# Optimization experiments

Hardware: AMD Instinct MI355X
Metric: run time of the kernel (lower is better)

## Reference

```python
import jax, jax.numpy as jnp
import numpy as np
import math

# dims
BSZ, L, D = 2, 4096, 1024
EXPAND, DS, NH, NG, DC, CS = 2, 128, 32, 1, 4, 64
DI = EXPAND * D            # 2048
HP = DI // NH              # 64 headdim
D_IN_PROJ = 2 * DI + 2 * NG * DS + NH  # 4384
CONV_DIM = DI + 2 * NG * DS            # 2304
EPS = 1e-5


def setup_inputs() -> dict:
    key = jax.random.key(0)
    ks = jax.random.split(key, 10)
    u = jax.random.normal(ks[0], (BSZ, L, D), dtype=jnp.float32)
    W_in = jax.random.normal(ks[1], (D, D_IN_PROJ), dtype=jnp.float32) / math.sqrt(D)
    conv_w = jax.random.normal(ks[2], (CONV_DIM, DC), dtype=jnp.float32) / math.sqrt(DC)
    conv_b = jnp.zeros((CONV_DIM,), dtype=jnp.float32)
    # dt init as in module: dt ~ logspace(1e-3, 0.1), dt_bias = inv softplus
    dt = jnp.exp(jax.random.uniform(ks[3], (NH,)) * (math.log(0.1) - math.log(0.001)) + math.log(0.001))
    dt = jnp.clip(dt, 1e-4, None)
    dt_bias = dt + jnp.log(-jnp.expm1(-dt))
    A_log = jnp.log(jax.random.uniform(ks[4], (NH,), minval=1.0, maxval=16.0))
    norm_w = jnp.ones((DI,), dtype=jnp.float32)
    norm_b = jnp.zeros((DI,), dtype=jnp.float32)
    W_out = jax.random.normal(ks[5], (DI, D), dtype=jnp.float32) / math.sqrt(DI)
    return {"u": u, "W_in": W_in, "conv_w": conv_w, "conv_b": conv_b,
            "dt_bias": dt_bias, "A_log": A_log, "norm_w": norm_w,
            "norm_b": norm_b, "W_out": W_out}


def _segsum(x):
    # x: (..., l) -> (..., l, l), out[i,j] = sum_{j<t<=i} x[t], -inf above diag
    cs = jnp.cumsum(x, axis=-1)
    d = cs[..., :, None] - cs[..., None, :]
    n = x.shape[-1]
    mask = jnp.tril(jnp.ones((n, n), dtype=bool))
    return jnp.where(mask, d, -jnp.inf)


def _ssd(x, A, Bm, Cm):
    # x: (b,l,h,p) already scaled by dt; A: (b,l,h) = a*dt; Bm,Cm: (b,l,h,n)
    b, l, h, p = x.shape
    nc = l // CS
    x = x.reshape(b, nc, CS, h, p)
    A = A.reshape(b, nc, CS, h).transpose(0, 3, 1, 2)          # (b,h,c,s)
    Bm = Bm.reshape(b, nc, CS, h, -1)
    Cm = Cm.reshape(b, nc, CS, h, -1)
    A_cum = jnp.cumsum(A, axis=-1)                              # (b,h,c,s)
    Lmat = jnp.exp(_segsum(A))                                  # (b,h,c,s,s)
    # intra-chunk (diagonal block) output
    Yd = jnp.einsum('bclhn,bcshn,bhcls,bcshp->bclhp', Cm, Bm, Lmat, x)
    # per-chunk final states
    decay_states = jnp.exp(A_cum[..., -1:] - A_cum)             # (b,h,c,s)
    states = jnp.einsum('bcshn,bhcs,bcshp->bchpn', Bm, decay_states, x)
    # inter-chunk recurrence (parallel via segsum over chunk decays)
    A_chunk = jnp.pad(A_cum[..., -1], ((0, 0), (0, 0), (1, 0)))  # (b,h,c+1)
    decay_chunk = jnp.exp(_segsum(A_chunk))                      # (b,h,c+1,c+1)
    states0 = jnp.concatenate([jnp.zeros_like(states[:, :1]), states], axis=1)
    new_states = jnp.einsum('bhzc,bchpn->bzhpn', decay_chunk, states0)
    states_in = new_states[:, :-1]                               # (b,c,h,p,n)
    state_decay = jnp.exp(A_cum)                                 # (b,h,c,s)
    Yoff = jnp.einsum('bcshn,bchpn,bhcs->bcshp', Cm, states_in, state_decay)
    return (Yd + Yoff).reshape(b, l, h, p)


def _causal_dwconv(x, w, b):
    # x: (B,L,C), depthwise causal conv, kernel w: (C,K), bias b: (C,)
    k = w.shape[1]
    xp = jnp.pad(x, ((0, 0), (k - 1, 0), (0, 0)))
    seqlen = x.shape[1]
    out = b
    for i in range(k):  # small fixed kernel loop (K=4)
        out = out + xp[:, i:i + seqlen, :] * w[:, i]
    return out


def reference(u, W_in, conv_w, conv_b, dt_bias, A_log, norm_w, norm_b, W_out):
    b, l, _ = u.shape
    zxbcdt = u @ W_in                                  # (b,l,2*DI+2*NG*DS+NH)
    z = zxbcdt[..., :DI]
    xBC = zxbcdt[..., DI:DI + CONV_DIM]
    dt = jax.nn.softplus(zxbcdt[..., -NH:] + dt_bias)  # (b,l,h)
    A = -jnp.exp(A_log)                                # (h,)
    xBC = jax.nn.silu(_causal_dwconv(xBC, conv_w, conv_b))
    x = xBC[..., :DI].reshape(b, l, NH, HP)
    Bv = xBC[..., DI:DI + NG * DS].reshape(b, l, NG, DS)
    Cv = xBC[..., DI + NG * DS:].reshape(b, l, NG, DS)
    # broadcast groups to heads
    rep = NH // NG
    Bh = jnp.repeat(Bv, rep, axis=2)                   # (b,l,h,n)
    Ch = jnp.repeat(Cv, rep, axis=2)
    y = _ssd(x * dt[..., None], A * dt, Bh, Ch)        # (b,l,h,p)
    y = y.reshape(b, l, DI)
    y = y * jax.nn.silu(z)                             # gated
    mu = jnp.mean(y, axis=-1, keepdims=True)
    var = jnp.mean(jnp.square(y - mu), axis=-1, keepdims=True)
    y = (y - mu) * jax.lax.rsqrt(var + EPS) * norm_w + norm_b
    return y @ W_out
```

## Files before the change

### kernel.cpp

```cpp
#include <hip/hip_runtime.h>
#include <hip/hip_bf16.h>
#include <math.h>


namespace {

constexpr int kB   = 2;
constexpr int kL   = 4096;
constexpr int kDI  = 2048;
constexpr int kDS  = 128;
constexpr int kNH  = 32;
constexpr int kHP  = 64;
constexpr int kDC  = 4;
constexpr int kCS  = 64;
constexpr int kNC  = kL / kCS;
constexpr int kDProj   = 2 * kDI + 2 * kDS + kNH;
constexpr int kDProjP  = 4480;
constexpr int kConvDim = kDI + 2 * kDS;
constexpr int kRows = kB * kL;
constexpr float kEps = 1e-5f;
constexpr int kTS = 130;
constexpr int kWS = 68;

typedef __bf16 bf16x8 __attribute__((ext_vector_type(8)));
typedef float f32x4 __attribute__((ext_vector_type(4)));
typedef unsigned short ushort8 __attribute__((ext_vector_type(8)));

__device__ inline float bu2f(unsigned short u) {
  union { unsigned int i; float f; } x; x.i = ((unsigned int)u) << 16; return x.f;
}
__device__ inline unsigned short f2bu(float f) {
  __hip_bfloat16 h = __float2bfloat16(f);
  return *reinterpret_cast<unsigned short*>(&h);
}

__device__ inline void gld_lds16(const unsigned short* g, unsigned short* l) {
  __builtin_amdgcn_global_load_lds(
      (const __attribute__((address_space(1))) unsigned int*)g,
      (__attribute__((address_space(3))) unsigned int*)l, 16, 0, 0);
}

__global__ void prep_kernel(const float4* __restrict__ u4, ushort4* __restrict__ A1,
                            const float* __restrict__ W_in, unsigned short* __restrict__ Bt1,
                            const float* __restrict__ W_out, unsigned short* __restrict__ Bt2,
                            const float* __restrict__ norm_w, const float* __restrict__ norm_b,
                            float* __restrict__ t1, float* __restrict__ t2) {
  constexpr int kCastBlocks = kRows * 1024 / 4 / 256;
  constexpr int kT1X = kDProjP / 32;
  constexpr int kT1Blocks = kT1X * (1024 / 32);
  constexpr int kT2X = 1024 / 32;
  constexpr int kT2Blocks = kT2X * (2048 / 32);
  __shared__ float t[32][33];
  __shared__ float p1[4][64], p2[4][64];
  int bid = (int)blockIdx.x;
  const int tid = threadIdx.x;
  if (bid < kCastBlocks) {
    int i = bid * 256 + tid;
    float4 v = u4[i];
    ushort4 o;
    o.x = f2bu(v.x); o.y = f2bu(v.y); o.z = f2bu(v.z); o.w = f2bu(v.w);
    A1[i] = o;
    return;
  }
  bid -= kCastBlocks;
  if (bid < kT1Blocks + kT2Blocks) {
    const float* in;
    unsigned short* out;
    int R, C, bx, by;
    const float* scale;
    if (bid < kT1Blocks) {
      in = W_in; out = Bt1; R = 1024; C = kDProj; scale = nullptr;
      bx = bid % kT1X; by = bid / kT1X;
    } else {
      int r = bid - kT1Blocks;
      in = W_out; out = Bt2; R = 2048; C = 1024; scale = norm_w;
      bx = r % kT2X; by = r / kT2X;
    }
    const int c0 = bx * 32, r0 = by * 32;
    const int tx = tid & 31, ty = tid >> 5;
    for (int rr = ty; rr < 32; rr += 8) {
      int c = c0 + tx;
      float v = (c < C) ? in[(size_t)(r0 + rr) * C + c] : 0.f;
      if (scale) v *= scale[r0 + rr];
      t[rr][tx] = v;
    }
    __syncthreads();
    for (int cc = ty; cc < 32; cc += 8) {
      int orow = c0 + cc;
      out[(size_t)orow * R + r0 + tx] = f2bu(t[tx][cc]);
    }
    return;
  }
  bid -= kT1Blocks + kT2Blocks;
  {
    const int nl = tid & 63;
    const int ks = tid >> 6;
    const int n = bid * 64 + nl;
    float s1 = 0.f, s2 = 0.f;
    for (int k = ks * 512; k < ks * 512 + 512; k++) {
      float v = W_out[(size_t)k * 1024 + n];
      s1 += norm_w[k] * v;
      s2 += norm_b[k] * v;
    }
    p1[ks][nl] = s1; p2[ks][nl] = s2;
    __syncthreads();
    if (tid < 64) {
      t1[bid * 64 + tid] = p1[0][tid] + p1[1][tid] + p1[2][tid] + p1[3][tid];
      t2[bid * 64 + tid] = p2[0][tid] + p2[1][tid] + p2[2][tid] + p2[3][tid];
    }
  }
}

__global__ __launch_bounds__(256, 4) void gemm_in(const unsigned short* __restrict__ A,
                                                  const unsigned short* __restrict__ Bt,
                                                  unsigned short* __restrict__ C,
                                                  int M, int N, int K) {
  __shared__ __align__(16) unsigned short As[128 * 64];
  __shared__ __align__(16) unsigned short Bs[128 * 64];
  const int tid = threadIdx.x;
  const int wave = tid >> 6, lane = tid & 63;
  const int nwg = (int)(gridDim.x * gridDim.y);
  const int orig = (int)(blockIdx.y * gridDim.x + blockIdx.x);
  const int swz = (orig & 7) * (nwg >> 3) + (orig >> 3);
  const int bx = swz % (int)gridDim.x, by = swz / (int)gridDim.x;
  const int m0 = by * 128, n0 = bx * 128;
  const int wr = (wave >> 1) * 64, wc = (wave & 1) * 64;
  const int l8 = lane >> 3, s8 = lane & 7;
  const unsigned short* pA[4];
  const unsigned short* pB[4];
  unsigned short* lA[4];
  unsigned short* lB[4];
#pragma unroll
  for (int r = 0; r < 4; r++) {
    int q = wave * 4 + r;
    pA[r] = A + (size_t)(m0 + q * 8 + l8) * K + (s8 ^ l8) * 8;
    pB[r] = Bt + (size_t)(n0 + q * 8 + l8) * K + (s8 ^ l8) * 8;
    lA[r] = &As[q * 512];
    lB[r] = &Bs[q * 512];
  }
  const int fr = lane & 15;
  const int c4 = lane >> 4;
  const int sk0 = (c4 ^ (fr & 7)) * 8;
  const int sk1 = ((4 | c4) ^ (fr & 7)) * 8;
  f32x4 acc[4][4] = {};
  for (int k0 = 0; k0 < K; k0 += 64) {
#pragma unroll
    for (int r = 0; r < 4; r++) {
      gld_lds16(pA[r] + k0, lA[r]);
      gld_lds16(pB[r] + k0, lB[r]);
    }
    asm volatile("s_waitcnt vmcnt(0)" ::: "memory");
    __syncthreads();
    {
      bf16x8 af0[4], bf0[4];
#pragma unroll
      for (int i = 0; i < 4; i++) {
        af0[i] = *(const bf16x8*)&As[(wr + i * 16 + fr) * 64 + sk0];
        bf0[i] = *(const bf16x8*)&Bs[(wc + i * 16 + fr) * 64 + sk0];
      }
#pragma unroll
      for (int i = 0; i < 4; i++)
#pragma unroll
        for (int j = 0; j < 4; j++)
          acc[i][j] = __builtin_amdgcn_mfma_f32_16x16x32_bf16(af0[i], bf0[j], acc[i][j], 0, 0, 0);
    }
    {
      bf16x8 af1[4], bf1[4];
#pragma unroll
      for (int i = 0; i < 4; i++) {
        af1[i] = *(const bf16x8*)&As[(wr + i * 16 + fr) * 64 + sk1];
        bf1[i] = *(const bf16x8*)&Bs[(wc + i * 16 + fr) * 64 + sk1];
      }
#pragma unroll
      for (int i = 0; i < 4; i++)
#pragma unroll
        for (int j = 0; j < 4; j++)
          acc[i][j] = __builtin_amdgcn_mfma_f32_16x16x32_bf16(af1[i], bf1[j], acc[i][j], 0, 0, 0);
    }
    __syncthreads();
  }
  const int crow = (lane >> 4) * 4;
  const int ccol = lane & 15;
#pragma unroll
  for (int i = 0; i < 4; i++) {
#pragma unroll
    for (int j = 0; j < 4; j++) {
      int n = n0 + wc + j * 16 + ccol;
      if (n < N) {
#pragma unroll
        for (int r = 0; r < 4; r++) {
          int m = m0 + wr + i * 16 + crow + r;
          C[(size_t)m * N + n] = f2bu(acc[i][j][r]);
        }
      }
    }
  }
}

__global__ __launch_bounds__(256, 4) void gemm_fold(const unsigned short* __restrict__ A,
                                                    const unsigned short* __restrict__ Bt,
                                                    float* __restrict__ C, int M, int N, int K,
                                                    const float* __restrict__ pS,
                                                    const float* __restrict__ pQ,
                                                    const float* __restrict__ t1,
                                                    const float* __restrict__ t2) {
  __shared__ __align__(16) unsigned short As[64 * 64];
  __shared__ __align__(16) unsigned short Bs[128 * 64];
  __shared__ float smu[64], srstd[64];
  const int tid = threadIdx.x;
  const int wave = tid >> 6, lane = tid & 63;
  const int nwg = (int)(gridDim.x * gridDim.y);
  const int orig = (int)(blockIdx.y * gridDim.x + blockIdx.x);
  const int swz = (orig & 7) * (nwg >> 3) + (orig >> 3);
  const int bx = swz % (int)gridDim.x, by = swz / (int)gridDim.x;
  const int m0 = by * 64, n0 = bx * 128;
  if (tid < 64) {
    int row = m0 + tid;
    float s = 0.f, q = 0.f;
#pragma unroll
    for (int i = 0; i < 8; i++) { s += pS[(size_t)row * 8 + i]; q += pQ[(size_t)row * 8 + i]; }
    float mval = s / kDI;
    smu[tid] = mval;
    srstd[tid] = rsqrtf(q / kDI - mval * mval + kEps);
  }
  const int wr = (wave >> 1) * 32, wc = (wave & 1) * 64;
  const int l8 = lane >> 3, s8 = lane & 7;
  const unsigned short* pA[2];
  const unsigned short* pB[4];
  unsigned short* lA[2];
  unsigned short* lB[4];
#pragma unroll
  for (int r = 0; r < 2; r++) {
    int q = wave * 2 + r;
    pA[r] = A + (size_t)(m0 + q * 8 + l8) * K + (s8 ^ l8) * 8;
    lA[r] = &As[q * 512];
  }
#pragma unroll
  for (int r = 0; r < 4; r++) {
    int q = wave * 4 + r;
    pB[r] = Bt + (size_t)(n0 + q * 8 + l8) * K + (s8 ^ l8) * 8;
    lB[r] = &Bs[q * 512];
  }
  const int fr = lane & 15;
  const int c4 = lane >> 4;
  const int sk0 = (c4 ^ (fr & 7)) * 8;
  const int sk1 = ((4 | c4) ^ (fr & 7)) * 8;
  f32x4 acc[2][4] = {};
  for (int k0 = 0; k0 < K; k0 += 64) {
#pragma unroll
    for (int r = 0; r < 2; r++) gld_lds16(pA[r] + k0, lA[r]);
#pragma unroll
    for (int r = 0; r < 4; r++) gld_lds16(pB[r] + k0, lB[r]);
    asm volatile("s_waitcnt vmcnt(0)" ::: "memory");
    __syncthreads();
    {
      bf16x8 af0[2], bf0[4];
#pragma unroll
      for (int i = 0; i < 2; i++)
        af0[i] = *(const bf16x8*)&As[(wr + i * 16 + fr) * 64 + sk0];
#pragma unroll
      for (int j = 0; j < 4; j++)
        bf0[j] = *(const bf16x8*)&Bs[(wc + j * 16 + fr) * 64 + sk0];
#pragma unroll
      for (int i = 0; i < 2; i++)
#pragma unroll
        for (int j = 0; j < 4; j++)
          acc[i][j] = __builtin_amdgcn_mfma_f32_16x16x32_bf16(af0[i], bf0[j], acc[i][j], 0, 0, 0);
    }
    {
      bf16x8 af1[2], bf1[4];
#pragma unroll
      for (int i = 0; i < 2; i++)
        af1[i] = *(const bf16x8*)&As[(wr + i * 16 + fr) * 64 + sk1];
#pragma unroll
      for (int j = 0; j < 4; j++)
        bf1[j] = *(const bf16x8*)&Bs[(wc + j * 16 + fr) * 64 + sk1];
#pragma unroll
      for (int i = 0; i < 2; i++)
#pragma unroll
        for (int j = 0; j < 4; j++)
          acc[i][j] = __builtin_amdgcn_mfma_f32_16x16x32_bf16(af1[i], bf1[j], acc[i][j], 0, 0, 0);
    }
    __syncthreads();
  }
  const int crow = (lane >> 4) * 4;
  const int ccol = lane & 15;
#pragma unroll
  for (int i = 0; i < 2; i++) {
#pragma unroll
    for (int j = 0; j < 4; j++) {
      int n = n0 + wc + j * 16 + ccol;
      float c1 = t1[n];
      float c2 = t2[n];
#pragma unroll
      for (int r = 0; r < 4; r++) {
        int ml = wr + i * 16 + crow + r;
        float v = acc[i][j][r];
        v = srstd[ml] * (v - smu[ml] * c1) + c2;
        C[(size_t)(m0 + ml) * N + n] = v;
      }
    }
  }
}

__global__ void conv_silu_kernel(const unsigned short* __restrict__ zxbcdt,
                                 const float* __restrict__ conv_w,
                                 const float* __restrict__ conv_b,
                                 unsigned short* __restrict__ xbc_act,
                                 const float* __restrict__ dt_bias,
                                 float* __restrict__ dtb) {
  const int r0 = blockIdx.y * 8;
  if (blockIdx.x == 0) {
    for (int e = threadIdx.x; e < 8 * kNH; e += 192) {
      int rr = r0 + (e >> 5), h = e & 31;
      float x = bu2f(zxbcdt[(size_t)rr * kDProj + (kDProj - kNH) + h]) + dt_bias[h];
      dtb[(size_t)rr * kNH + h] = (x > 15.f) ? x : log1pf(expf(x));
    }
  }
  int c4 = blockIdx.x * 192 + threadIdx.x;
  if (c4 >= kConvDim / 4) return;
  const int c = c4 * 4;
  const int l0 = r0 & (kL - 1);
  float4 w[4];
  float bias[4];
#pragma unroll
  for (int q = 0; q < 4; q++) {
    w[q] = ((const float4*)conv_w)[c + q];
    bias[q] = conv_b[c + q];
  }
  float v[11][4];
#pragma unroll
  for (int i = 0; i < 11; i++) {
    int l = l0 - 3 + i;
    if (l >= 0) {
      ushort4 t = *(const ushort4*)&zxbcdt[(size_t)(r0 - 3 + i) * kDProj + kDI + c];
      v[i][0] = bu2f(t.x); v[i][1] = bu2f(t.y); v[i][2] = bu2f(t.z); v[i][3] = bu2f(t.w);
    } else {
      v[i][0] = v[i][1] = v[i][2] = v[i][3] = 0.f;
    }
  }
#pragma unroll
  for (int j = 0; j < 8; j++) {
    ushort4 o;
    unsigned short* op = (unsigned short*)&o;
#pragma unroll
    for (int q = 0; q < 4; q++) {
      float a = bias[q] + v[j][q] * w[q].x + v[j + 1][q] * w[q].y +
                v[j + 2][q] * w[q].z + v[j + 3][q] * w[q].w;
      op[q] = f2bu(a / (1.f + expf(-a)));
    }
    *(ushort4*)&xbc_act[(size_t)(r0 + j) * kConvDim + c] = o;
  }
}

__global__ __launch_bounds__(256) void chunk_state_kernel(
    const unsigned short* __restrict__ xbc_act,
    const float* __restrict__ dtbuf,
    const float* __restrict__ A_log,
    unsigned short* __restrict__ states,
    float* __restrict__ asum) {
  const int id = blockIdx.x;
  const int h = id & 31;
  const int c = (id >> 5) & (kNC - 1);
  const int b = id >> 11;
  const int tid = threadIdx.x;
  const int wave = tid >> 6, lane = tid & 63;
  __shared__ __align__(16) unsigned short sBT[kDS * kWS];
  __shared__ __align__(16) unsigned short sxd[kCS * kWS];
  __shared__ float s_dt[kCS];
  __shared__ float s_acum[kCS];
  const int l0 = b * kL + c * kCS;
  if (tid < kCS) s_dt[tid] = dtbuf[(size_t)(l0 + tid) * kNH + h];
  __syncthreads();
  if (tid < 64) {
    float A = -expf(A_log[h]);
    float v = A * s_dt[tid];
#pragma unroll
    for (int off = 1; off < 64; off <<= 1) {
      float u = __shfl_up(v, off);
      if (tid >= off) v += u;
    }
    s_acum[tid] = v;
    if (tid == 63) asum[id] = v;
  }
  __syncthreads();
  const float total = s_acum[kCS - 1];
  for (int e = tid; e < kCS * kDS; e += 256) {
    int s = e >> 7, n = e & 127;
    sBT[n * kWS + s] = xbc_act[(size_t)(l0 + s) * kConvDim + kDI + n];
  }
  for (int e = tid; e < kCS * kHP; e += 256) {
    int s = e >> 6, p = e & 63;
    float xv = bu2f(xbc_act[(size_t)(l0 + s) * kConvDim + h * kHP + p]);
    sxd[p * kWS + s] = f2bu(xv * s_dt[s] * expf(total - s_acum[s]));
  }
  __syncthreads();
  const int arow = wave * 16 + (lane & 15);
  const int fk = (lane >> 4) * 8;
  f32x4 acc[8] = {};
#pragma unroll
  for (int kk = 0; kk < 2; kk++) {
    bf16x8 a = *(const bf16x8*)&sxd[arow * kWS + kk * 32 + fk];
#pragma unroll
    for (int j = 0; j < 8; j++) {
      bf16x8 bb = *(const bf16x8*)&sBT[(j * 16 + (lane & 15)) * kWS + kk * 32 + fk];
      acc[j] = __builtin_amdgcn_mfma_f32_16x16x32_bf16(a, bb, acc[j], 0, 0, 0);
    }
  }
  const int prow = wave * 16 + (lane >> 4) * 4;
  const int ncol = lane & 15;
  size_t base = (size_t)id * (kHP * kDS);
#pragma unroll
  for (int j = 0; j < 8; j++)
#pragma unroll
    for (int r = 0; r < 4; r++)
      states[base + (size_t)(prow + r) * kDS + j * 16 + ncol] = f2bu(acc[j][r]);
}

__global__ void scan_kernel(unsigned short* __restrict__ states,
                            const float* __restrict__ asum) {
  const int blk = blockIdx.x;
  const int seg = blk & 15;
  const int bh = blk >> 4;
  const int h = bh & 31, b = bh >> 5;
  const int e2 = seg * 256 + threadIdx.x;
  const size_t cs = (size_t)kNH * 4096;
  ushort2* p = (ushort2*)states + ((size_t)(b * kNC) * kNH + h) * 4096 + e2;
  const float* ap = asum + (b * kNC) * kNH + h;
  float c0 = 0.f, c1 = 0.f;
  ushort2 t0 = p[0];
  ushort2 t1v = p[cs];
  ushort2 t2v = p[2 * cs];
  ushort2 t3v = p[3 * cs];
  float d0 = expf(ap[0]);
  float d1 = expf(ap[kNH]);
  float d2 = expf(ap[2 * kNH]);
  float d3 = expf(ap[3 * kNH]);
  for (int g = 0; g < kNC; g += 4) {
    ushort2 n0 = t0, n1 = t1v, n2 = t2v, n3 = t3v;
    float e0 = d0, e1 = d1, e2f = d2, e3 = d3;
    if (g + 4 < kNC) {
      n0 = p[(size_t)(g + 4) * cs]; e0 = expf(ap[(g + 4) * kNH]);
      n1 = p[(size_t)(g + 5) * cs]; e1 = expf(ap[(g + 5) * kNH]);
      n2 = p[(size_t)(g + 6) * cs]; e2f = expf(ap[(g + 6) * kNH]);
      n3 = p[(size_t)(g + 7) * cs]; e3 = expf(ap[(g + 7) * kNH]);
    }
    ushort2 o;
    o.x = f2bu(c0); o.y = f2bu(c1); p[(size_t)g * cs] = o;
    c0 = c0 * d0 + bu2f(t0.x); c1 = c1 * d0 + bu2f(t0.y);
    o.x = f2bu(c0); o.y = f2bu(c1); p[(size_t)(g + 1) * cs] = o;
    c0 = c0 * d1 + bu2f(t1v.x); c1 = c1 * d1 + bu2f(t1v.y);
    o.x = f2bu(c0); o.y = f2bu(c1); p[(size_t)(g + 2) * cs] = o;
    c0 = c0 * d2 + bu2f(t2v.x); c1 = c1 * d2 + bu2f(t2v.y);
    o.x = f2bu(c0); o.y = f2bu(c1); p[(size_t)(g + 3) * cs] = o;
    c0 = c0 * d3 + bu2f(t3v.x); c1 = c1 * d3 + bu2f(t3v.y);
    t0 = n0; t1v = n1; t2v = n2; t3v = n3;
    d0 = e0; d1 = e1; d2 = e2f; d3 = e3;
  }
}

__global__ __launch_bounds__(256) void y_kernel(
    const unsigned short* __restrict__ xbc_act,
    const unsigned short* __restrict__ zxbcdt,
    const unsigned short* __restrict__ states_in,
    const float* __restrict__ dtbuf,
    const float* __restrict__ A_log,
    unsigned short* __restrict__ ybuf,
    float* __restrict__ pS, float* __restrict__ pQ) {
  const int id = blockIdx.x;
  const int hg = id & 7;
  const int c = (id >> 3) & (kNC - 1);
  const int b = id >> 9;
  const int tid = threadIdx.x;
  const int wave = tid >> 6, lane = tid & 63;
  __shared__ __align__(16) unsigned short sC[kCS * kTS];
  __shared__ __align__(16) unsigned short sB[kCS * kTS];
  __shared__ __align__(16) unsigned short sxd[kCS * kWS];
  __shared__ __align__(16) unsigned short sW[kCS * kWS];
  __shared__ float s_dt[4][kCS];
  __shared__ float s_acum[4][kCS];
  const int l0 = b * kL + c * kCS;
  {
    int hh = tid >> 6, s = tid & 63;
    s_dt[hh][s] = dtbuf[(size_t)(l0 + s) * kNH + hg * 4 + hh];
  }
  __syncthreads();
  {
    int hh = tid >> 6, s = tid & 63;
    float A = -expf(A_log[hg * 4 + hh]);
    float v = A * s_dt[hh][s];
#pragma unroll
    for (int off = 1; off < 64; off <<= 1) {
      float u = __shfl_up(v, off);
      if (s >= off) v += u;
    }
    s_acum[hh][s] = v;
  }
  for (int e = tid; e < kCS * 16; e += 256) {
    int row = e >> 4, c8 = (e & 15) * 8;
    size_t rb = (size_t)(l0 + row) * kConvDim;
    *(ushort8*)&sB[row * kTS + c8] = *(const ushort8*)&xbc_act[rb + kDI + c8];
    *(ushort8*)&sC[row * kTS + c8] = *(const ushort8*)&xbc_act[rb + kDI + kDS + c8];
  }
  __syncthreads();
  const int arow = wave * 16 + (lane & 15);
  const int fk = (lane >> 4) * 8;
  f32x4 accG[4] = {};
#pragma unroll
  for (int kk = 0; kk < 4; kk++) {
    bf16x8 a = *(const bf16x8*)&sC[arow * kTS + kk * 32 + fk];
#pragma unroll
    for (int j = 0; j < 4; j++) {
      bf16x8 bb = *(const bf16x8*)&sB[(j * 16 + (lane & 15)) * kTS + kk * 32 + fk];
      accG[j] = __builtin_amdgcn_mfma_f32_16x16x32_bf16(a, bb, accG[j], 0, 0, 0);
    }
  }
  const int lrow = wave * 16 + (lane >> 4) * 4;
  const size_t sbase = (size_t)((b * kNC + c) * kNH) * (kHP * kDS);
  float rS[4] = {}, rQ[4] = {};
  for (int hh = 0; hh < 4; hh++) {
    const int h = hg * 4 + hh;
    __syncthreads();
    for (int e = tid; e < kCS * kHP; e += 256) {
      int s = e >> 6, p = e & 63;
      float xv = bu2f(xbc_act[(size_t)(l0 + s) * kConvDim + h * kHP + p]);
      sxd[p * kWS + s] = f2bu(xv * s_dt[hh][s]);
    }
#pragma unroll
    for (int j = 0; j < 4; j++) {
      int scol = j * 16 + (lane & 15);
      float as = s_acum[hh][scol];
#pragma unroll
      for (int r = 0; r < 4; r++) {
        int l = lrow + r;
        float w = (scol <= l) ? accG[j][r] * expf(s_acum[hh][l] - as) : 0.f;
        sW[l * kWS + scol] = f2bu(w);
      }
    }
    for (int e = tid; e < kCS * 16; e += 256) {
      int row = e >> 4, c8 = (e & 15) * 8;
      *(ushort8*)&sB[row * kTS + c8] =
          *(const ushort8*)&states_in[sbase + (size_t)h * (kHP * kDS) + row * kDS + c8];
    }
    __syncthreads();
    f32x4 accY[4] = {};
#pragma unroll
    for (int kk = 0; kk < 2; kk++) {
      bf16x8 a = *(const bf16x8*)&sW[arow * kWS + kk * 32 + fk];
#pragma unroll
      for (int j = 0; j < 4; j++) {
        bf16x8 bb = *(const bf16x8*)&sxd[(j * 16 + (lane & 15)) * kWS + kk * 32 + fk];
        accY[j] = __builtin_amdgcn_mfma_f32_16x16x32_bf16(a, bb, accY[j], 0, 0, 0);
      }
    }
    f32x4 accO[4] = {};
#pragma unroll
    for (int kk = 0; kk < 4; kk++) {
      bf16x8 a = *(const bf16x8*)&sC[arow * kTS + kk * 32 + fk];
#pragma unroll
      for (int j = 0; j < 4; j++) {
        bf16x8 bb = *(const bf16x8*)&sB[(j * 16 + (lane & 15)) * kTS + kk * 32 + fk];
        accO[j] = __builtin_amdgcn_mfma_f32_16x16x32_bf16(a, bb, accO[j], 0, 0, 0);
      }
    }
#pragma unroll
    for (int r = 0; r < 4; r++) {
      int l = lrow + r;
      float el = expf(s_acum[hh][l]);
      size_t zrow = (size_t)(l0 + l) * kDProj + h * kHP;
      size_t yrow = (size_t)(l0 + l) * kDI + h * kHP;
#pragma unroll
      for (int j = 0; j < 4; j++) {
        int p = j * 16 + (lane & 15);
        float yv = accY[j][r] + el * accO[j][r];
        float z = bu2f(zxbcdt[zrow + p]);
        yv *= z / (1.f + expf(-z));
        rS[r] += yv;
        rQ[r] += yv * yv;
        ybuf[yrow + p] = f2bu(yv);
      }
    }
  }
#pragma unroll
  for (int m = 1; m < 16; m <<= 1) {
#pragma unroll
    for (int r = 0; r < 4; r++) {
      rS[r] += __shfl_xor(rS[r], m);
      rQ[r] += __shfl_xor(rQ[r], m);
    }
  }
  if ((lane & 15) == 0) {
#pragma unroll
    for (int r = 0; r < 4; r++) {
      int row = l0 + lrow + r;
      pS[(size_t)row * 8 + hg] = rS[r];
      pQ[(size_t)row * 8 + hg] = rQ[r];
    }
  }
}

}

extern "C" void kernel_launch(void* const* d_in, const int* in_sizes, int n_in,
                              void* d_out, int out_size, void* d_ws, size_t ws_size,
                              hipStream_t stream) {
  const float* u       = (const float*)d_in[0];
  const float* W_in    = (const float*)d_in[1];
  const float* conv_w  = (const float*)d_in[2];
  const float* conv_b  = (const float*)d_in[3];
  const float* dt_bias = (const float*)d_in[4];
  const float* A_log   = (const float*)d_in[5];
  const float* norm_w  = (const float*)d_in[6];
  const float* norm_b  = (const float*)d_in[7];
  const float* W_out   = (const float*)d_in[8];
  float* out = (float*)d_out;

  char* ws = (char*)d_ws;
  size_t off = 0;
  auto alloc = [&](size_t bytes) {
    void* p = ws + off;
    off += (bytes + 255) & ~(size_t)255;
    return p;
  };
  unsigned short* zxbcdt = (unsigned short*)alloc((size_t)kRows * kDProj * 2);
  unsigned short* xbc    = (unsigned short*)alloc((size_t)kRows * kConvDim * 2);
  float* dtb             = (float*)alloc((size_t)kRows * kNH * 4);
  float* asum            = (float*)alloc((size_t)kB * kNC * kNH * 4);
  unsigned short* A1     = (unsigned short*)alloc((size_t)kRows * 1024 * 2);
  unsigned short* Bt1    = (unsigned short*)alloc((size_t)kDProjP * 1024 * 2);
  unsigned short* states = (unsigned short*)alloc((size_t)kB * kNC * kNH * kHP * kDS * 2);
  unsigned short* Bt2    = (unsigned short*)alloc((size_t)1024 * kDI * 2);
  unsigned short* ybuf   = (unsigned short*)alloc((size_t)kRows * kDI * 2);
  float* t1              = (float*)alloc(1024 * 4);
  float* t2              = (float*)alloc(1024 * 4);
  float* pS              = (float*)alloc((size_t)kRows * 8 * 4);
  float* pQ              = (float*)alloc((size_t)kRows * 8 * 4);
  (void)ws_size; (void)in_sizes; (void)n_in; (void)out_size;

  constexpr int kPrepBlocks = kRows * 1024 / 4 / 256
                            + (kDProjP / 32) * (1024 / 32)
                            + (1024 / 32) * (2048 / 32)
                            + 16;
  prep_kernel<<<kPrepBlocks, 256, 0, stream>>>(
      (const float4*)u, (ushort4*)A1, W_in, Bt1, W_out, Bt2, norm_w, norm_b, t1, t2);
  gemm_in<<<dim3(kDProjP / 128, kRows / 128), 256, 0, stream>>>(
      A1, Bt1, zxbcdt, kRows, kDProj, 1024);
  conv_silu_kernel<<<dim3(3, kRows / 8), 192, 0, stream>>>(zxbcdt, conv_w, conv_b, xbc,
                                                           dt_bias, dtb);
  chunk_state_kernel<<<kB * kNC * kNH, 256, 0, stream>>>(xbc, dtb, A_log, states, asum);
  scan_kernel<<<kB * kNH * 16, 256, 0, stream>>>(states, asum);
  y_kernel<<<kB * kNC * 8, 256, 0, stream>>>(xbc, zxbcdt, states, dtb, A_log, ybuf, pS, pQ);
  gemm_fold<<<dim3(1024 / 128, kRows / 64), 256, 0, stream>>>(
      ybuf, Bt2, out, kRows, 1024, 2048, pS, pQ, t1, t2);
}
```

Measured before the change: 410.8 us.

## Process eight heads per chunk-state block reusing B tile; split input GEMM

The chunk_state kernel now handles 8 heads per block instead of one. The B tile is loaded into shared memory once and reused across all 8 heads, and the scaled x tile is double-buffered so the next head's data is prepared while the current head's MFMA runs. This cuts redundant global reads of B but reduces the grid from 4096 to 512 blocks and serialises the head loop. The input-projection GEMM is also split into two launches over row halves, which adds launch overhead and has no obvious reuse benefit.

Result: slower. 435.2 us (+5.9%).

```diff
diff --git a/kernel.cpp b/kernel.cpp
--- a/kernel.cpp
+++ b/kernel.cpp
@@ -360,61 +360,83 @@
     unsigned short* __restrict__ states,
     float* __restrict__ asum) {
   const int id = blockIdx.x;
-  const int h = id & 31;
-  const int c = (id >> 5) & (kNC - 1);
-  const int b = id >> 11;
+  const int hg = id & 3;
+  const int c = (id >> 2) & (kNC - 1);
+  const int b = id >> 8;
+  const int h0 = hg * 8;
   const int tid = threadIdx.x;
   const int wave = tid >> 6, lane = tid & 63;
   __shared__ __align__(16) unsigned short sBT[kDS * kWS];
-  __shared__ __align__(16) unsigned short sxd[kCS * kWS];
-  __shared__ float s_dt[kCS];
-  __shared__ float s_acum[kCS];
+  __shared__ __align__(16) unsigned short sxd[2][kCS * kWS];
+  __shared__ float s_dt[8][kCS];
+  __shared__ float s_acum[8][kCS];
   const int l0 = b * kL + c * kCS;
-  if (tid < kCS) s_dt[tid] = dtbuf[(size_t)(l0 + tid) * kNH + h];
+  const int bc = b * kNC + c;
+  for (int e = tid; e < 8 * kCS; e += 256) {
+    int hh = e >> 6, s = e & 63;
+    s_dt[hh][s] = dtbuf[(size_t)(l0 + s) * kNH + h0 + hh];
+  }
   __syncthreads();
-  if (tid < 64) {
-    float A = -expf(A_log[h]);
-    float v = A * s_dt[tid];
+#pragma unroll
+  for (int pass = 0; pass < 2; pass++) {
+    int hh = wave + pass * 4;
+    float A = -expf(A_log[h0 + hh]);
+    float v = A * s_dt[hh][lane];
 #pragma unroll
     for (int off = 1; off < 64; off <<= 1) {
       float u = __shfl_up(v, off);
-      if (tid >= off) v += u;
-    }
-    s_acum[tid] = v;
-    if (tid == 63) asum[id] = v;
-  }
-  __syncthreads();
-  const float total = s_acum[kCS - 1];
+      if (lane >= off) v += u;
+    }
+    s_acum[hh][lane] = v;
+    if (lane == 63) asum[(size_t)bc * kNH + h0 + hh] = v;
+  }
   for (int e = tid; e < kCS * kDS; e += 256) {
     int s = e >> 7, n = e & 127;
     sBT[n * kWS + s] = xbc_act[(size_t)(l0 + s) * kConvDim + kDI + n];
   }
-  for (int e = tid; e < kCS * kHP; e += 256) {
-    int s = e >> 6, p = e & 63;
-    float xv = bu2f(xbc_act[(size_t)(l0 + s) * kConvDim + h * kHP + p]);
-    sxd[p * kWS + s] = f2bu(xv * s_dt[s] * expf(total - s_acum[s]));
+  __syncthreads();
+  {
+    const float total = s_acum[0][kCS - 1];
+    for (int e = tid; e < kCS * kHP; e += 256) {
+      int s = e >> 6, p = e & 63;
+      float xv = bu2f(xbc_act[(size_t)(l0 + s) * kConvDim + h0 * kHP + p]);
+      sxd[0][p * kWS + s] = f2bu(xv * s_dt[0][s] * expf(total - s_acum[0][s]));
+    }
   }
   __syncthreads();
   const int arow = wave * 16 + (lane & 15);
   const int fk = (lane >> 4) * 8;
-  f32x4 acc[8] = {};
-#pragma unroll
-  for (int kk = 0; kk < 2; kk++) {
-    bf16x8 a = *(const bf16x8*)&sxd[arow * kWS + kk * 32 + fk];
-#pragma unroll
-    for (int j = 0; j < 8; j++) {
-      bf16x8 bb = *(const bf16x8*)&sBT[(j * 16 + (lane & 15)) * kWS + kk * 32 + fk];
-      acc[j] = __builtin_amdgcn_mfma_f32_16x16x32_bf16(a, bb, acc[j], 0, 0, 0);
-    }
-  }
   const int prow = wave * 16 + (lane >> 4) * 4;
   const int ncol = lane & 15;
-  size_t base = (size_t)id * (kHP * kDS);
-#pragma unroll
-  for (int j = 0; j < 8; j++)
-#pragma unroll
-    for (int r = 0; r < 4; r++)
-      states[base + (size_t)(prow + r) * kDS + j * 16 + ncol] = f2bu(acc[j][r]);
+  for (int hh = 0; hh < 8; hh++) {
+    f32x4 acc[8] = {};
+#pragma unroll
+    for (int kk = 0; kk < 2; kk++) {
+      bf16x8 a = *(const bf16x8*)&sxd[hh & 1][arow * kWS + kk * 32 + fk];
+#pragma unroll
+      for (int j = 0; j < 8; j++) {
+        bf16x8 bb = *(const bf16x8*)&sBT[(j * 16 + (lane & 15)) * kWS + kk * 32 + fk];
+        acc[j] = __builtin_amdgcn_mfma_f32_16x16x32_bf16(a, bb, acc[j], 0, 0, 0);
+      }
+    }
+    if (hh < 7) {
+      const int hn = h0 + hh + 1;
+      const float total = s_acum[hh + 1][kCS - 1];
+      for (int e = tid; e < kCS * kHP; e += 256) {
+        int s = e >> 6, p = e & 63;
+        float xv = bu2f(xbc_act[(size_t)(l0 + s) * kConvDim + hn * kHP + p]);
+        sxd[(hh + 1) & 1][p * kWS + s] =
+            f2bu(xv * s_dt[hh + 1][s] * expf(total - s_acum[hh + 1][s]));
+      }
+    }
+    size_t base = ((size_t)bc * kNH + h0 + hh) * (kHP * kDS);
+#pragma unroll
+    for (int j = 0; j < 8; j++)
+#pragma unroll
+      for (int r = 0; r < 4; r++)
+        states[base + (size_t)(prow + r) * kDS + j * 16 + ncol] = f2bu(acc[j][r]);
+    __syncthreads();
+  }
 }
 
 __global__ void scan_kernel(unsigned short* __restrict__ states,
@@ -643,11 +665,14 @@
                             + 16;
   prep_kernel<<<kPrepBlocks, 256, 0, stream>>>(
       (const float4*)u, (ushort4*)A1, W_in, Bt1, W_out, Bt2, norm_w, norm_b, t1, t2);
-  gemm_in<<<dim3(kDProjP / 128, kRows / 128), 256, 0, stream>>>(
-      A1, Bt1, zxbcdt, kRows, kDProj, 1024);
+  gemm_in<<<dim3(kDProjP / 128, kRows / 256), 256, 0, stream>>>(
+      A1, Bt1, zxbcdt, kRows / 2, kDProj, 1024);
+  gemm_in<<<dim3(kDProjP / 128, kRows / 256), 256, 0, stream>>>(
+      A1 + (size_t)(kRows / 2) * 1024, Bt1, zxbcdt + (size_t)(kRows / 2) * kDProj,
+      kRows / 2, kDProj, 1024);
   conv_silu_kernel<<<dim3(3, kRows / 8), 192, 0, stream>>>(zxbcdt, conv_w, conv_b, xbc,
                                                            dt_bias, dtb);
-  chunk_state_kernel<<<kB * kNC * kNH, 256, 0, stream>>>(xbc, dtb, A_log, states, asum);
+  chunk_state_kernel<<<kB * kNC * 4, 256, 0, stream>>>(xbc, dtb, A_log, states, asum);
   scan_kernel<<<kB * kNH * 16, 256, 0, stream>>>(states, asum);
   y_kernel<<<kB * kNC * 8, 256, 0, stream>>>(xbc, zxbcdt, states, dtb, A_log, ybuf, pS, pQ);
   gemm_fold<<<dim3(1024 / 128, kRows / 64), 256, 0, stream>>>(
```
